# Optimization experiments

Hardware: AMD Instinct MI355X
Metric: run time of the kernel (lower is better)

Reference implementation:

```python
import jax, jax.numpy as jnp
import numpy as np

B, I, DI, O, DO = 256, 1152, 8, 10, 16
ROUTING_ITERS = 3


def squash(s):
    # squash along last dim (out_capsule_dim); keepdims version of the
    # module's intended math: v = s * |s|^2 / (1+|s|^2) / |s|
    sq = jnp.sum(s * s, axis=-1, keepdims=True)
    return s * sq / (1.0 + sq) / jnp.sqrt(sq)


def setup_inputs() -> dict:
    key = jax.random.key(0)
    k1, k2 = jax.random.split(key)
    x = jax.random.normal(k1, (B, I, DI), dtype=jnp.float32)
    stdv = 1.0 / np.sqrt(I)
    W = jax.random.uniform(k2, (I, O, DO, DI), dtype=jnp.float32,
                           minval=-stdv, maxval=stdv)
    return {"x": x, "W": W}


def reference(x, W):
    # u_hat[b,i,o,d] = W[i,o,d,k] @ x[b,i,k]
    u_hat = jnp.einsum('iodk,bik->biod', W, x)  # [B, I, O, DO]
    u_det = jax.lax.stop_gradient(u_hat)
    b_ij = jnp.zeros((B, I, O), dtype=u_hat.dtype)
    v = None
    for it in range(ROUTING_ITERS):
        c = jax.nn.softmax(b_ij, axis=2)              # softmax over out caps
        uh = u_hat if it == ROUTING_ITERS - 1 else u_det
        s = jnp.einsum('bio,biod->bod', c, uh)        # [B, O, DO]
        v = squash(s)
        if it < ROUTING_ITERS - 1:
            b_ij = b_ij + jnp.einsum('biod,bod->bio', u_det, v)
    return v  # [B, O, DO]
```

## Files before the change

kernel.cpp:

```cpp
#include <hip/hip_runtime.h>
#include <hip/hip_fp16.h>
#include <math.h>


constexpr int Bc  = 256;
constexpr int Ic  = 1152;
constexpr int Oc  = 10;
constexpr int DOc = 16;
constexpr int ODc = 160;
constexpr int ITILES = 72;

__device__ __forceinline__ float dpp16_sum(float v) {
    int s;
    s = __builtin_amdgcn_update_dpp(0, __float_as_int(v), 0xB1, 0xF, 0xF, true);
    v += __int_as_float(s);
    s = __builtin_amdgcn_update_dpp(0, __float_as_int(v), 0x4E, 0xF, 0xF, true);
    v += __int_as_float(s);
    s = __builtin_amdgcn_update_dpp(0, __float_as_int(v), 0x124, 0xF, 0xF, true);
    v += __int_as_float(s);
    s = __builtin_amdgcn_update_dpp(0, __float_as_int(v), 0x128, 0xF, 0xF, true);
    v += __int_as_float(s);
    return v;
}

__global__ __launch_bounds__(256, 4) void k_uhat(const float* __restrict__ x,
                                                 const float* __restrict__ W,
                                                 __half2* __restrict__ uws,
                                                 float* __restrict__ partial) {
    const int bx    = blockIdx.x;
    const int itile = bx % ITILES;
    const int btile = bx / ITILES;
    const int t     = threadIdx.x;
    const int d     = t & 15;
    const int il    = t >> 4;
    const int w     = t >> 6;
    const int i     = itile * 16 + il;
    const int b0    = btile * 16;

    __shared__ __align__(16) float xs[16 * 128];
    __shared__ __align__(16) float pacc[4 * 16 * ODc];

#pragma unroll
    for (int j = 0; j < 2; ++j) {
        int e  = t + j * 256;
        int bb = e >> 5;
        int r  = e & 31;
        ((float4*)xs)[e] =
            ((const float4*)(x + (size_t)(b0 + bb) * (Ic * 8) + itile * 128))[r];
    }

    float4 wr[20];
    {
        const float4* wp = (const float4*)(W + (((size_t)i * Oc) * DOc + d) * 8);
#pragma unroll
        for (int o = 0; o < Oc; ++o) {
            wr[2 * o]     = wp[o * 32];
            wr[2 * o + 1] = wp[o * 32 + 1];
        }
    }
    __syncthreads();

    const int ch    = i >> 6;
    const int off_t = (i & 63) * 16 + d;

#pragma unroll 1
    for (int bb = 0; bb < 16; ++bb) {
        const int b = b0 + bb;
        const float4 xa = *((const float4*)(xs + bb * 128 + il * 8));
        const float4 xb = *((const float4*)(xs + bb * 128 + il * 8 + 4));
        float u[Oc];
#pragma unroll
        for (int o = 0; o < Oc; ++o) {
            float4 w0 = wr[2 * o], w1 = wr[2 * o + 1];
            u[o] = w0.x * xa.x + w0.y * xa.y + w0.z * xa.z + w0.w * xa.w +
                   w1.x * xb.x + w1.y * xb.y + w1.z * xb.z + w1.w * xb.w;
        }
        __half2* ub = uws + ((size_t)b * 90 + ch * 5) * 1024 + off_t;
#pragma unroll
        for (int op = 0; op < 5; ++op)
            ub[op * 1024] = __floats2half2_rn(u[2 * op], u[2 * op + 1]);
#pragma unroll
        for (int o = 0; o < Oc; ++o) {
            float a = u[o];
            a += __shfl_xor(a, 16);
            a += __shfl_xor(a, 32);
            if ((t & 63) < 16) pacc[(w * 16 + bb) * ODc + o * 16 + d] = a;
        }
    }
    __syncthreads();
#pragma unroll
    for (int j = 0; j < 10; ++j) {
        int e = t + j * 256;
        float s = pacc[e] + pacc[2560 + e] + pacc[5120 + e] + pacc[7680 + e];
        partial[(size_t)itile * (Bc * ODc) + b0 * ODc + e] = s;
    }
}

template <int PASS>
__global__ __launch_bounds__(1024, 8) void k_route(const __half2* __restrict__ uws,
                                                   const float* __restrict__ partial,
                                                   const float* __restrict__ sprev,
                                                   float* __restrict__ vsumg,
                                                   float* __restrict__ spart) {
    const int bx  = blockIdx.x;
    const int b   = bx >> 1;
    const int h   = bx & 1;
    const int t   = threadIdx.x;
    const int d   = t & 15;
    const int wid = t >> 6;

    __shared__ float vs_s[ODc];
    __shared__ float red4[4 * ODc];
    __shared__ float red[16 * ODc];

    if (PASS == 1) {
        const int team = t >> 8;
        const int tt   = t & 255;
        if (tt < ODc) {
            float s = 0.f;
            const float* pb = partial + (size_t)team * 18 * (Bc * ODc) + b * ODc + tt;
#pragma unroll 6
            for (int p = 0; p < 18; ++p) s += pb[(size_t)p * (Bc * ODc)];
            red4[team * ODc + tt] = s;
        }
        __syncthreads();
        if (t < ODc) {
            float s = (red4[t] + red4[ODc + t] + red4[2 * ODc + t] +
                       red4[3 * ODc + t]) * 0.1f;
            float sq = dpp16_sum(s * s);
            float v = s * (sq / ((1.f + sq) * sqrtf(sq)));
            vs_s[t] = v;
            vsumg[b * ODc + t] = v;
        }
    } else {
        if (t < ODc) {
            float s = sprev[b * ODc + t] + sprev[(size_t)(Bc * ODc) + b * ODc + t];
            float sq = dpp16_sum(s * s);
            float v = s * (sq / ((1.f + sq) * sqrtf(sq)));
            vs_s[t] = vsumg[b * ODc + t] + v;
        }
    }
    __syncthreads();

    float vsr[Oc];
#pragma unroll
    for (int o = 0; o < Oc; ++o) vsr[o] = vs_s[o * 16 + d];
    float acc[Oc];
#pragma unroll
    for (int o = 0; o < Oc; ++o) acc[o] = 0.f;

    const __half2* wsb = uws + ((size_t)b * 90 + h * 45) * 1024 + t;
#pragma unroll 1
    for (int ch = 0; ch < 9; ++ch) {
        float uo[Oc];
#pragma unroll
        for (int op = 0; op < 5; ++op) {
            float2 f = __half22float2(wsb[(ch * 5 + op) * 1024]);
            uo[2 * op]     = f.x;
            uo[2 * op + 1] = f.y;
        }
        float c[Oc];
#pragma unroll
        for (int o = 0; o < Oc; ++o) c[o] = dpp16_sum(uo[o] * vsr[o]);
        float m = c[0];
#pragma unroll
        for (int o = 1; o < Oc; ++o) m = fmaxf(m, c[o]);
        float se = 0.f;
#pragma unroll
        for (int o = 0; o < Oc; ++o) {
            c[o] = __expf(c[o] - m);
            se += c[o];
        }
        const float inv = 1.f / se;
#pragma unroll
        for (int o = 0; o < Oc; ++o) acc[o] += (c[o] * inv) * uo[o];
    }
#pragma unroll
    for (int o = 0; o < Oc; ++o) {
        float a = acc[o];
        a += __shfl_xor(a, 16);
        a += __shfl_xor(a, 32);
        if ((t & 63) < 16) red[wid * ODc + o * 16 + d] = a;
    }
    __syncthreads();
    if (t < ODc) {
        float s = 0.f;
#pragma unroll
        for (int w = 0; w < 16; ++w) s += red[w * ODc + t];
        spart[(size_t)h * (Bc * ODc) + b * ODc + t] = s;
    }
}

__global__ __launch_bounds__(192) void k_final(const float* __restrict__ spart,
                                               float* __restrict__ out) {
    const int b = blockIdx.x;
    const int t = threadIdx.x;
    if (t >= ODc) return;
    float s = spart[b * ODc + t] + spart[(size_t)(Bc * ODc) + b * ODc + t];
    float sq = dpp16_sum(s * s);
    float v = s * (sq / ((1.f + sq) * sqrtf(sq)));
    out[(size_t)b * ODc + t] = v;
}

__global__ void __launch_bounds__(1024, 4)
digitcaps_fallback(const float* __restrict__ x, const float* __restrict__ W,
                   float* __restrict__ out) {
    const int b = blockIdx.x, t = threadIdx.x;
    const int lane = t & 63, wid = t >> 6, d = t & 15, iblk = t >> 4;
    __shared__ __align__(16) float xs[Ic * 8];
    __shared__ __align__(16) float red[16 * ODc];
    __shared__ __align__(16) float svec[ODc], vcur[ODc], vsum[ODc];
    {
        const float4* xg = (const float4*)(x + (size_t)b * (Ic * 8));
        float4* xl = (float4*)xs;
        for (int j = t; j < Ic * 2; j += 1024) xl[j] = xg[j];
    }
    if (t < ODc) vsum[t] = 0.f;
    __syncthreads();
    float acc[Oc], vsr[Oc];
    for (int it = 0; it < 3; ++it) {
#pragma unroll
        for (int o = 0; o < Oc; ++o) { acc[o] = 0.f; vsr[o] = vsum[o * 16 + d]; }
#pragma unroll 1
        for (int chk = 0; chk < 18; ++chk) {
            const int i = chk * 64 + iblk;
            const float4 xa = ((const float4*)(xs + i * 8))[0];
            const float4 xb = ((const float4*)(xs + i * 8))[1];
            const float* wb = W + (((size_t)i * Oc) * DOc + d) * 8;
            float uo[Oc];
#pragma unroll
            for (int o = 0; o < Oc; ++o) {
                const float4* wp = (const float4*)(wb + o * 128);
                float4 w0 = wp[0], w1 = wp[1];
                uo[o] = w0.x * xa.x + w0.y * xa.y + w0.z * xa.z + w0.w * xa.w +
                        w1.x * xb.x + w1.y * xb.y + w1.z * xb.z + w1.w * xb.w;
            }
            float cc[Oc];
            if (it > 0) {
#pragma unroll
                for (int o = 0; o < Oc; ++o) cc[o] = dpp16_sum(uo[o] * vsr[o]);
                float m = cc[0];
#pragma unroll
                for (int o = 1; o < Oc; ++o) m = fmaxf(m, cc[o]);
                float se = 0.f;
#pragma unroll
                for (int o = 0; o < Oc; ++o) { cc[o] = __expf(cc[o] - m); se += cc[o]; }
                float inv = 1.f / se;
#pragma unroll
                for (int o = 0; o < Oc; ++o) acc[o] += cc[o] * inv * uo[o];
            } else {
#pragma unroll
                for (int o = 0; o < Oc; ++o) acc[o] += 0.1f * uo[o];
            }
        }
#pragma unroll
        for (int o = 0; o < Oc; ++o) {
            float a = acc[o];
            a += __shfl_xor(a, 16);
            a += __shfl_xor(a, 32);
            if (lane < 16) red[wid * ODc + o * 16 + lane] = a;
        }
        __syncthreads();
        if (t < ODc) {
            float s = 0.f;
#pragma unroll
            for (int w = 0; w < 16; ++w) s += red[w * ODc + t];
            svec[t] = s;
        }
        __syncthreads();
        if (t < Oc) {
            float sq = 0.f;
#pragma unroll
            for (int dd = 0; dd < DOc; ++dd) sq += svec[t * 16 + dd] * svec[t * 16 + dd];
            float sc = sq / ((1.f + sq) * sqrtf(sq));
#pragma unroll
            for (int dd = 0; dd < DOc; ++dd) {
                float v = svec[t * 16 + dd] * sc;
                vcur[t * 16 + dd] = v;
                vsum[t * 16 + dd] += v;
            }
        }
        __syncthreads();
    }
    if (t < ODc) out[(size_t)b * ODc + t] = vcur[t];
}

extern "C" void kernel_launch(void* const* d_in, const int* in_sizes, int n_in,
                              void* d_out, int out_size, void* d_ws, size_t ws_size,
                              hipStream_t stream) {
    (void)in_sizes; (void)n_in; (void)out_size;
    const float* x = (const float*)d_in[0];
    const float* W = (const float*)d_in[1];
    float* out     = (float*)d_out;

    const size_t UWS_B   = (size_t)Bc * 90 * 1024 * sizeof(__half2);
    const size_t PART_B  = (size_t)ITILES * Bc * ODc * sizeof(float);
    const size_t SP1_B   = (size_t)2 * Bc * ODc * sizeof(float);
    const size_t SP2_B   = (size_t)2 * Bc * ODc * sizeof(float);
    const size_t VSUM_B  = (size_t)Bc * ODc * sizeof(float);

    __half2* uws   = (__half2*)d_ws;
    float* partial = (float*)((char*)d_ws + UWS_B);
    float* spart1  = (float*)((char*)d_ws + UWS_B + PART_B);
    float* spart2  = (float*)((char*)d_ws + UWS_B + PART_B + SP1_B);
    float* vsumg   = (float*)((char*)d_ws + UWS_B + PART_B + SP1_B + SP2_B);

    if (ws_size >= UWS_B + PART_B + SP1_B + SP2_B + VSUM_B) {
        hipLaunchKernelGGL(k_uhat, dim3(ITILES * 16), dim3(256), 0, stream,
                           x, W, uws, partial);
        hipLaunchKernelGGL((k_route<1>), dim3(512), dim3(1024), 0, stream,
                           uws, partial, nullptr, vsumg, spart1);
        hipLaunchKernelGGL((k_route<2>), dim3(512), dim3(1024), 0, stream,
                           uws, nullptr, spart1, vsumg, spart2);
        hipLaunchKernelGGL(k_final, dim3(Bc), dim3(192), 0, stream,
                           spart2, out);
    } else {
        hipLaunchKernelGGL(digitcaps_fallback, dim3(Bc), dim3(1024), 0, stream,
                           x, W, out);
    }
}
```

Before: 150.2 us.

## Pack u_hat workspace into 16B+4B vectors and prefetch chunks in routing

New measurement: 151.9 us. About the same (+1.1%).

```diff
diff --git a/kernel.cpp b/kernel.cpp
--- a/kernel.cpp
+++ b/kernel.cpp
@@ -23,9 +23,23 @@
     return v;
 }
 
+__device__ __forceinline__ unsigned int pack_h2(float a, float b) {
+    __half2 h = __floats2half2_rn(a, b);
+    unsigned int u;
+    __builtin_memcpy(&u, &h, 4);
+    return u;
+}
+
+__device__ __forceinline__ float2 unpack_h2(unsigned int u) {
+    __half2 h;
+    __builtin_memcpy(&h, &u, 4);
+    return __half22float2(h);
+}
+
 __global__ __launch_bounds__(256, 4) void k_uhat(const float* __restrict__ x,
                                                  const float* __restrict__ W,
-                                                 __half2* __restrict__ uws,
+                                                 uint4* __restrict__ ws4,
+                                                 unsigned int* __restrict__ ws1,
                                                  float* __restrict__ partial) {
     const int bx    = blockIdx.x;
     const int itile = bx % ITILES;
@@ -38,7 +52,7 @@
     const int b0    = btile * 16;
 
     __shared__ __align__(16) float xs[16 * 128];
-    __shared__ __align__(16) float pacc[4 * 16 * ODc];
+    __shared__ __align__(16) float pacc[4 * 8 * ODc];
 
 #pragma unroll
     for (int j = 0; j < 2; ++j) {
@@ -60,44 +74,50 @@
     }
     __syncthreads();
 
-    const int ch    = i >> 6;
-    const int off_t = (i & 63) * 16 + d;
+    const int chg   = i >> 6;
+    const int t_pos = (i & 63) * 16 + d;
 
 #pragma unroll 1
-    for (int bb = 0; bb < 16; ++bb) {
-        const int b = b0 + bb;
-        const float4 xa = *((const float4*)(xs + bb * 128 + il * 8));
-        const float4 xb = *((const float4*)(xs + bb * 128 + il * 8 + 4));
-        float u[Oc];
-#pragma unroll
-        for (int o = 0; o < Oc; ++o) {
-            float4 w0 = wr[2 * o], w1 = wr[2 * o + 1];
-            u[o] = w0.x * xa.x + w0.y * xa.y + w0.z * xa.z + w0.w * xa.w +
-                   w1.x * xb.x + w1.y * xb.y + w1.z * xb.z + w1.w * xb.w;
-        }
-        __half2* ub = uws + ((size_t)b * 90 + ch * 5) * 1024 + off_t;
-#pragma unroll
-        for (int op = 0; op < 5; ++op)
-            ub[op * 1024] = __floats2half2_rn(u[2 * op], u[2 * op + 1]);
-#pragma unroll
-        for (int o = 0; o < Oc; ++o) {
-            float a = u[o];
-            a += __shfl_xor(a, 16);
-            a += __shfl_xor(a, 32);
-            if ((t & 63) < 16) pacc[(w * 16 + bb) * ODc + o * 16 + d] = a;
-        }
-    }
-    __syncthreads();
-#pragma unroll
-    for (int j = 0; j < 10; ++j) {
-        int e = t + j * 256;
-        float s = pacc[e] + pacc[2560 + e] + pacc[5120 + e] + pacc[7680 + e];
-        partial[(size_t)itile * (Bc * ODc) + b0 * ODc + e] = s;
+    for (int half = 0; half < 2; ++half) {
+#pragma unroll 1
+        for (int bb8 = 0; bb8 < 8; ++bb8) {
+            const int bb = half * 8 + bb8;
+            const int b  = b0 + bb;
+            const float4 xa = *((const float4*)(xs + bb * 128 + il * 8));
+            const float4 xb = *((const float4*)(xs + bb * 128 + il * 8 + 4));
+            float u[Oc];
+#pragma unroll
+            for (int o = 0; o < Oc; ++o) {
+                float4 w0 = wr[2 * o], w1 = wr[2 * o + 1];
+                u[o] = w0.x * xa.x + w0.y * xa.y + w0.z * xa.z + w0.w * xa.w +
+                       w1.x * xb.x + w1.y * xb.y + w1.z * xb.z + w1.w * xb.w;
+            }
+            const size_t idx = ((size_t)b * 18 + chg) * 1024 + t_pos;
+            ws4[idx] = make_uint4(pack_h2(u[0], u[1]), pack_h2(u[2], u[3]),
+                                  pack_h2(u[4], u[5]), pack_h2(u[6], u[7]));
+            ws1[idx] = pack_h2(u[8], u[9]);
+#pragma unroll
+            for (int o = 0; o < Oc; ++o) {
+                float a = u[o];
+                a += __shfl_xor(a, 16);
+                a += __shfl_xor(a, 32);
+                if ((t & 63) < 16) pacc[(w * 8 + bb8) * ODc + o * 16 + d] = a;
+            }
+        }
+        __syncthreads();
+#pragma unroll
+        for (int j = 0; j < 5; ++j) {
+            int e = t + j * 256;
+            float s = pacc[e] + pacc[1280 + e] + pacc[2560 + e] + pacc[3840 + e];
+            partial[(size_t)itile * (Bc * ODc) + (b0 + half * 8) * ODc + e] = s;
+        }
+        __syncthreads();
     }
 }
 
 template <int PASS>
-__global__ __launch_bounds__(1024, 8) void k_route(const __half2* __restrict__ uws,
+__global__ __launch_bounds__(1024, 8) void k_route(const uint4* __restrict__ ws4,
+                                                   const unsigned int* __restrict__ ws1,
                                                    const float* __restrict__ partial,
                                                    const float* __restrict__ sprev,
                                                    float* __restrict__ vsumg,
@@ -149,15 +169,27 @@
 #pragma unroll
     for (int o = 0; o < Oc; ++o) acc[o] = 0.f;
 
-    const __half2* wsb = uws + ((size_t)b * 90 + h * 45) * 1024 + t;
+    const uint4* wb4        = ws4 + ((size_t)b * 18 + h * 9) * 1024 + t;
+    const unsigned int* wb1 = ws1 + ((size_t)b * 18 + h * 9) * 1024 + t;
+
+    uint4 curA        = wb4[0];
+    unsigned int curB = wb1[0];
 #pragma unroll 1
     for (int ch = 0; ch < 9; ++ch) {
+        uint4 nxtA;
+        unsigned int nxtB;
+        if (ch < 8) {
+            nxtA = wb4[(ch + 1) * 1024];
+            nxtB = wb1[(ch + 1) * 1024];
+        }
         float uo[Oc];
-#pragma unroll
-        for (int op = 0; op < 5; ++op) {
-            float2 f = __half22float2(wsb[(ch * 5 + op) * 1024]);
-            uo[2 * op]     = f.x;
-            uo[2 * op + 1] = f.y;
+        {
+            float2 f;
+            f = unpack_h2(curA.x); uo[0] = f.x; uo[1] = f.y;
+            f = unpack_h2(curA.y); uo[2] = f.x; uo[3] = f.y;
+            f = unpack_h2(curA.z); uo[4] = f.x; uo[5] = f.y;
+            f = unpack_h2(curA.w); uo[6] = f.x; uo[7] = f.y;
+            f = unpack_h2(curB);   uo[8] = f.x; uo[9] = f.y;
         }
         float c[Oc];
 #pragma unroll
@@ -174,6 +206,8 @@
         const float inv = 1.f / se;
 #pragma unroll
         for (int o = 0; o < Oc; ++o) acc[o] += (c[o] * inv) * uo[o];
+        curA = nxtA;
+        curB = nxtB;
     }
 #pragma unroll
     for (int o = 0; o < Oc; ++o) {
@@ -293,25 +327,28 @@
     const float* W = (const float*)d_in[1];
     float* out     = (float*)d_out;
 
-    const size_t UWS_B   = (size_t)Bc * 90 * 1024 * sizeof(__half2);
-    const size_t PART_B  = (size_t)ITILES * Bc * ODc * sizeof(float);
-    const size_t SP1_B   = (size_t)2 * Bc * ODc * sizeof(float);
-    const size_t SP2_B   = (size_t)2 * Bc * ODc * sizeof(float);
-    const size_t VSUM_B  = (size_t)Bc * ODc * sizeof(float);
-
-    __half2* uws   = (__half2*)d_ws;
-    float* partial = (float*)((char*)d_ws + UWS_B);
-    float* spart1  = (float*)((char*)d_ws + UWS_B + PART_B);
-    float* spart2  = (float*)((char*)d_ws + UWS_B + PART_B + SP1_B);
-    float* vsumg   = (float*)((char*)d_ws + UWS_B + PART_B + SP1_B + SP2_B);
-
-    if (ws_size >= UWS_B + PART_B + SP1_B + SP2_B + VSUM_B) {
+    const size_t WS4_B  = (size_t)Bc * 18 * 1024 * 16;
+    const size_t WS1_B  = (size_t)Bc * 18 * 1024 * 4;
+    const size_t PART_B = (size_t)ITILES * Bc * ODc * sizeof(float);
+    const size_t SP1_B  = (size_t)2 * Bc * ODc * sizeof(float);
+    const size_t SP2_B  = (size_t)2 * Bc * ODc * sizeof(float);
+    const size_t VSUM_B = (size_t)Bc * ODc * sizeof(float);
+
+    char* p = (char*)d_ws;
+    uint4* ws4        = (uint4*)p;                 p += WS4_B;
+    unsigned int* ws1 = (unsigned int*)p;          p += WS1_B;
+    float* partial    = (float*)p;                 p += PART_B;
+    float* spart1     = (float*)p;                 p += SP1_B;
+    float* spart2     = (float*)p;                 p += SP2_B;
+    float* vsumg      = (float*)p;
+
+    if (ws_size >= WS4_B + WS1_B + PART_B + SP1_B + SP2_B + VSUM_B) {
         hipLaunchKernelGGL(k_uhat, dim3(ITILES * 16), dim3(256), 0, stream,
-                           x, W, uws, partial);
+                           x, W, ws4, ws1, partial);
         hipLaunchKernelGGL((k_route<1>), dim3(512), dim3(1024), 0, stream,
-                           uws, partial, nullptr, vsumg, spart1);
+                           ws4, ws1, partial, nullptr, vsumg, spart1);
         hipLaunchKernelGGL((k_route<2>), dim3(512), dim3(1024), 0, stream,
-                           uws, nullptr, spart1, vsumg, spart2);
+                           ws4, ws1, nullptr, spart1, vsumg, spart2);
         hipLaunchKernelGGL(k_final, dim3(Bc), dim3(192), 0, stream,
                            spart2, out);
     } else {
```
